# Kernel optimization log

Measured on AMD Instinct MI355X. Metric: run time of the kernel, lower is better.

## Reference

```python
import jax, jax.numpy as jnp
import numpy as np

B, N, H, M = 1, 1024, 64, 32


def _posenc(n, d):
    # sinusoidal positional encoding, matches torch PositionalEncoding (eval mode, no dropout)
    pos = jnp.arange(n, dtype=jnp.float32)[:, None]
    div = jnp.exp(jnp.arange(0, d, 2, dtype=jnp.float32) * (-np.log(10000.0) / d))
    ang = pos * div  # [n, d//2]
    pe = jnp.zeros((n, d), jnp.float32)
    pe = pe.at[:, 0::2].set(jnp.sin(ang))
    pe = pe.at[:, 1::2].set(jnp.cos(ang))
    return pe


def _egnn(x, h, m2f, w_msg, b_msg, w_pos, b_pos, w_feat, b_feat):
    # x: [B,N,3], h: [B,N,Hd], m2f: [B,N,N] float pair mask (diag zero)
    Bn, Nn, Hd = h.shape
    m2 = m2f[..., None]
    # r[b,i,j] = x[b,j] - x[b,i]  (torch: x.unsqueeze(-3) - x.unsqueeze(-2))
    r = (x[:, None, :, :] - x[:, :, None, :]) * m2  # [B,N,N,3]
    d2 = jnp.sum(r * r, axis=-1)  # [B,N,N]
    # message_mlp(cat(hi, hj, d2)): hi[b,i,j]=h[j], hj[b,i,j]=h[i]
    # split weight to avoid materializing the N x N x (2H+1) concat
    Wa, Wb, wd = w_msg[:, :Hd], w_msg[:, Hd:2 * Hd], w_msg[:, 2 * Hd]
    A = h @ Wa.T   # [B,N,M], contribution of h_j (hi slot)
    Bm = h @ Wb.T  # [B,N,M], contribution of h_i (hj slot)
    m = jax.nn.relu(A[:, None, :, :] + Bm[:, :, None, :] + d2[..., None] * wd + b_msg) * m2  # [B,N,N,M]
    mx = (m @ w_pos.T + b_pos) * r  # [B,N,N,3]
    x = x + jnp.sum(mx, axis=-2) / (Nn - 1)
    msum = jnp.sum(m, axis=-2)  # [B,N,M]
    h = jnp.concatenate([h, msum], axis=-1) @ w_feat.T + b_feat  # [B,N,Hd]
    return x, h


def setup_inputs() -> dict:
    key = jax.random.key(0)
    ks = jax.random.split(key, 16)
    def lin_w(k, o, i):
        return (jax.random.normal(k, (o, i), jnp.float32) / np.sqrt(i)).astype(jnp.float32)
    def lin_b(k, o):
        return (jax.random.normal(k, (o,), jnp.float32) * 0.02).astype(jnp.float32)
    return {
        'positions': jax.random.normal(ks[0], (B, N, 3), jnp.float32),
        'features': jax.random.normal(ks[1], (B, N, H), jnp.float32),
        'mask': jnp.ones((B, N), dtype=bool),
        'w_msg1': lin_w(ks[2], M, 2 * H + 1), 'b_msg1': lin_b(ks[3], M),
        'w_pos1': lin_w(ks[4], 3, M), 'b_pos1': lin_b(ks[5], 3),
        'w_feat1': lin_w(ks[6], H, M + H), 'b_feat1': lin_b(ks[7], H),
        'w_msg2': lin_w(ks[8], M, 2 * H + 1), 'b_msg2': lin_b(ks[9], M),
        'w_pos2': lin_w(ks[10], 3, M), 'b_pos2': lin_b(ks[11], 3),
        'w_feat2': lin_w(ks[12], H, M + H), 'b_feat2': lin_b(ks[13], H),
        't': 0,
    }


def reference(positions, features, mask,
              w_msg1, b_msg1, w_pos1, b_pos1, w_feat1, b_feat1,
              w_msg2, b_msg2, w_pos2, b_pos2, w_feat2, b_feat2, t):
    Bn, Nn, Hd = features.shape
    h = features + _posenc(Nn, Hd)[None]
    mask2 = mask[:, None, :] & mask[:, :, None]
    mask2 = mask2 & (~jnp.eye(Nn, dtype=bool))[None]  # zero self-pairs
    m2f = mask2.astype(positions.dtype)
    x = positions
    x, h = _egnn(x, h, m2f, w_msg1, b_msg1, w_pos1, b_pos1, w_feat1, b_feat1)
    h = jax.nn.relu(h)
    x, h = _egnn(x, h, m2f, w_msg2, b_msg2, w_pos2, b_pos2, w_feat2, b_feat2)
    return x
```

## Files before the change

### kernel.cpp

```cpp
#include <hip/hip_runtime.h>

#define N    1024
#define HD   64
#define MD   32
#define BLK  256
#define BLKP 512
#define WROW (2 * HD + 1)

typedef _Float16 h2 __attribute__((ext_vector_type(2)));

__device__ __forceinline__ float dot2(h2 a, h2 b, float c)
{
#if __has_builtin(__builtin_amdgcn_fdot2)
    return __builtin_amdgcn_fdot2(a, b, c, false);
#else
    return c + (float)a[0] * (float)b[0] + (float)a[1] * (float)b[1];
#endif
}
__device__ __forceinline__ h2 pack2(float x, float y)
{
    h2 r; r[0] = (_Float16)x; r[1] = (_Float16)y; return r;
}

__global__ __launch_bounds__(BLK) void k_p0(const float* __restrict__ feat,
                                            const float* __restrict__ wmsg,
                                            const float* __restrict__ bmsg,
                                            float* __restrict__ h0,
                                            float* __restrict__ A,
                                            float* __restrict__ Bb,
                                            _Float16* __restrict__ Ah)
{
    __shared__ float scr[4160 + 4 * HD];
    const int tid = threadIdx.x;
    const int n0  = blockIdx.x * 4;

    for (int u = tid; u < MD * WROW; u += BLK) scr[u] = wmsg[u];
    float* hrow = scr + 4160;
    {
        const int n = n0 + (tid >> 6), d = tid & 63;
        const float div = expf((float)(d & ~1) * (-9.210340371976184f / 64.0f));
        const float ang = (float)n * div;
        const float pe  = (d & 1) ? cosf(ang) : sinf(ang);
        const float hv  = feat[n * HD + d] + pe;
        h0[n * HD + d] = hv;
        hrow[tid] = hv;
    }
    __syncthreads();
    if (tid < 4 * MD) {
        const int nl = tid >> 5, m = tid & 31;
        const float* wa = scr + m * WROW;
        const float* hr = hrow + nl * HD;
        float sa = 0.f, sb = bmsg[m];
#pragma unroll
        for (int c = 0; c < HD; c++) {
            const float hv = hr[c];
            sa = fmaf(hv, wa[c], sa);
            sb = fmaf(hv, wa[HD + c], sb);
        }
        const int n = n0 + nl;
        A[n * MD + m]  = sa;
        Bb[n * MD + m] = sb;
        Ah[n * MD + m] = (_Float16)sa;
    }
}

template<int LAYER1>
__global__ __launch_bounds__(BLKP) void k_pair(
    const float* __restrict__ xsrc, const float* __restrict__ Aap,
    const _Float16* __restrict__ Ahp, const float* __restrict__ Bbp,
    const float* __restrict__ wmsg, const float* __restrict__ wpos,
    const float* __restrict__ bpos, float* __restrict__ xout,
    const float* __restrict__ h0, const float* __restrict__ wf,
    const float* __restrict__ bf, const float* __restrict__ wmsg2,
    const float* __restrict__ bmsg2, float* __restrict__ A2,
    float* __restrict__ B2, _Float16* __restrict__ A2h)
{
    const int tid   = threadIdx.x;
    const int wid   = tid >> 6;
    const int lane  = tid & 63;
    const int kq    = lane & 3;
    const int jslot = lane >> 2;

    __shared__ float  sbuf[6848];
    __shared__ float  wacc[8][8];
    __shared__ float  msAl[8][MD];
    __shared__ float  msBl[8][MD];
    __shared__ float  SxL[3];
    __shared__ float  msF[2][MD];
    __shared__ float  h0r[2][HD];
    __shared__ float  h1r[2][HD];
    float4* rd = (float4*)sbuf;

    const int iA = blockIdx.x, iB = blockIdx.x + N / 2;
    const float xiA0 = xsrc[iA * 3 + 0], xiA1 = xsrc[iA * 3 + 1], xiA2 = xsrc[iA * 3 + 2];
    const float xiB0 = xsrc[iB * 3 + 0], xiB1 = xsrc[iB * 3 + 1], xiB2 = xsrc[iB * 3 + 2];
    const float dx0 = xiA0 - xiB0, dx1 = xiA1 - xiB1, dx2 = xiA2 - xiB2;

    float sx0 = 0.f, sx1 = 0.f, sx2 = 0.f;
#pragma unroll
    for (int q = 0; q < N / BLKP; q++) {
        const int j = q * BLKP + tid;
        const float xj0 = xsrc[j * 3 + 0];
        const float xj1 = xsrc[j * 3 + 1];
        const float xj2 = xsrc[j * 3 + 2];
        sx0 += xj0; sx1 += xj1; sx2 += xj2;
        const float a0 = xj0 - xiA0, a1 = xj1 - xiA1, a2 = xj2 - xiA2;
        const float d2A = fmaf(a0, a0, fmaf(a1, a1, a2 * a2));
        const float b0 = xj0 - xiB0, b1 = xj1 - xiB1, b2 = xj2 - xiB2;
        const float d2B = fmaf(b0, b0, fmaf(b1, b1, b2 * b2));
        rd[j] = make_float4(a0, a1, a2, __builtin_bit_cast(float, pack2(d2A, d2B)));
    }
#pragma unroll
    for (int off = 32; off > 0; off >>= 1) {
        sx0 += __shfl_xor(sx0, off);
        sx1 += __shfl_xor(sx1, off);
        sx2 += __shfl_xor(sx2, off);
    }
    if (lane == 0) { wacc[wid][0] = sx0; wacc[wid][1] = sx1; wacc[wid][2] = sx2; }
    __syncthreads();
    if (tid == 0) {
        float s0 = 0.f, s1 = 0.f, s2 = 0.f;
#pragma unroll
        for (int w = 0; w < 8; w++) { s0 += wacc[w][0]; s1 += wacc[w][1]; s2 += wacc[w][2]; }
        SxL[0] = s0; SxL[1] = s1; SxL[2] = s2;
    }

    h2 biA[4], biB[4], wpx[4], wpy[4], wpz[4], wd[4];
    {
        const float4 bA0 = *(const float4*)(Bbp + iA * MD + kq * 8);
        const float4 bA1 = *(const float4*)(Bbp + iA * MD + kq * 8 + 4);
        const float4 bB0 = *(const float4*)(Bbp + iB * MD + kq * 8);
        const float4 bB1 = *(const float4*)(Bbp + iB * MD + kq * 8 + 4);
        biA[0] = pack2(bA0.x, bA0.y); biA[1] = pack2(bA0.z, bA0.w);
        biA[2] = pack2(bA1.x, bA1.y); biA[3] = pack2(bA1.z, bA1.w);
        biB[0] = pack2(bB0.x, bB0.y); biB[1] = pack2(bB0.z, bB0.w);
        biB[2] = pack2(bB1.x, bB1.y); biB[3] = pack2(bB1.z, bB1.w);
        const float4 px0 = *(const float4*)(wpos + kq * 8);
        const float4 px1 = *(const float4*)(wpos + kq * 8 + 4);
        const float4 py0 = *(const float4*)(wpos + MD + kq * 8);
        const float4 py1 = *(const float4*)(wpos + MD + kq * 8 + 4);
        const float4 pz0 = *(const float4*)(wpos + 2 * MD + kq * 8);
        const float4 pz1 = *(const float4*)(wpos + 2 * MD + kq * 8 + 4);
        wpx[0] = pack2(px0.x, px0.y); wpx[1] = pack2(px0.z, px0.w);
        wpx[2] = pack2(px1.x, px1.y); wpx[3] = pack2(px1.z, px1.w);
        wpy[0] = pack2(py0.x, py0.y); wpy[1] = pack2(py0.z, py0.w);
        wpy[2] = pack2(py1.x, py1.y); wpy[3] = pack2(py1.z, py1.w);
        wpz[0] = pack2(pz0.x, pz0.y); wpz[1] = pack2(pz0.z, pz0.w);
        wpz[2] = pack2(pz1.x, pz1.y); wpz[3] = pack2(pz1.z, pz1.w);
#pragma unroll
        for (int t = 0; t < 4; t++)
            wd[t] = pack2(wmsg[(kq * 8 + 2 * t) * WROW + 2 * HD],
                          wmsg[(kq * 8 + 2 * t + 1) * WROW + 2 * HD]);
    }
    const h2 hz = pack2(0.f, 0.f);

    float aA0 = 0.f, aA1 = 0.f, aA2 = 0.f, aB0 = 0.f, aB1 = 0.f, aB2 = 0.f;
    h2 msA[4] = {hz, hz, hz, hz}, msB[4] = {hz, hz, hz, hz};

    const int jb = wid * (N / 8);
#pragma unroll 8
    for (int it = 0; it < 8; it++) {
        const int j = jb + it * 16 + jslot;
        const uint4 au = *(const uint4*)(Ahp + j * MD + kq * 8);
        h2 a[4];
        a[0] = __builtin_bit_cast(h2, au.x); a[1] = __builtin_bit_cast(h2, au.y);
        a[2] = __builtin_bit_cast(h2, au.z); a[3] = __builtin_bit_cast(h2, au.w);
        const float4 f = rd[j];
        const h2 dd = __builtin_bit_cast(h2, f.w);
        const h2 dA = __builtin_shufflevector(dd, dd, 0, 0);
        const h2 dB = __builtin_shufflevector(dd, dd, 1, 1);
        const float rB0 = f.x + dx0, rB1 = f.y + dx1, rB2 = f.z + dx2;

        h2 mA[4], mB[4];
#pragma unroll
        for (int t = 0; t < 4; t++) {
            mA[t] = __builtin_elementwise_max(dA * wd[t] + (a[t] + biA[t]), hz);
            mB[t] = __builtin_elementwise_max(dB * wd[t] + (a[t] + biB[t]), hz);
            if (LAYER1) { msA[t] += mA[t]; msB[t] += mB[t]; }
        }
        const float sAx = dot2(mA[3], wpx[3], dot2(mA[2], wpx[2], dot2(mA[1], wpx[1], dot2(mA[0], wpx[0], 0.f))));
        const float sAy = dot2(mA[3], wpy[3], dot2(mA[2], wpy[2], dot2(mA[1], wpy[1], dot2(mA[0], wpy[0], 0.f))));
        const float sAz = dot2(mA[3], wpz[3], dot2(mA[2], wpz[2], dot2(mA[1], wpz[1], dot2(mA[0], wpz[0], 0.f))));
        const float sBx = dot2(mB[3], wpx[3], dot2(mB[2], wpx[2], dot2(mB[1], wpx[1], dot2(mB[0], wpx[0], 0.f))));
        const float sBy = dot2(mB[3], wpy[3], dot2(mB[2], wpy[2], dot2(mB[1], wpy[1], dot2(mB[0], wpy[0], 0.f))));
        const float sBz = dot2(mB[3], wpz[3], dot2(mB[2], wpz[2], dot2(mB[1], wpz[1], dot2(mB[0], wpz[0], 0.f))));
        aA0 = fmaf(sAx, f.x, aA0);
        aA1 = fmaf(sAy, f.y, aA1);
        aA2 = fmaf(sAz, f.z, aA2);
        aB0 = fmaf(sBx, rB0, aB0);
        aB1 = fmaf(sBy, rB1, aB1);
        aB2 = fmaf(sBz, rB2, aB2);
    }

#pragma unroll
    for (int off = 32; off > 0; off >>= 1) {
        aA0 += __shfl_xor(aA0, off); aA1 += __shfl_xor(aA1, off); aA2 += __shfl_xor(aA2, off);
        aB0 += __shfl_xor(aB0, off); aB1 += __shfl_xor(aB1, off); aB2 += __shfl_xor(aB2, off);
    }
    float msAf[8], msBf[8];
    if (LAYER1) {
#pragma unroll
        for (int t = 0; t < 4; t++) {
            msAf[2 * t] = (float)msA[t][0]; msAf[2 * t + 1] = (float)msA[t][1];
            msBf[2 * t] = (float)msB[t][0]; msBf[2 * t + 1] = (float)msB[t][1];
        }
#pragma unroll
        for (int off = 4; off <= 32; off <<= 1) {
#pragma unroll
            for (int t = 0; t < 8; t++) {
                msAf[t] += __shfl_xor(msAf[t], off);
                msBf[t] += __shfl_xor(msBf[t], off);
            }
        }
    }
    __syncthreads();
    if (lane == 0) {
        wacc[wid][0] = aA0; wacc[wid][1] = aA1; wacc[wid][2] = aA2;
        wacc[wid][3] = aB0; wacc[wid][4] = aB1; wacc[wid][5] = aB2;
    }
    if (LAYER1 && jslot == 0) {
#pragma unroll
        for (int t = 0; t < 8; t++) {
            msAl[wid][kq * 8 + t] = msAf[t];
            msBl[wid][kq * 8 + t] = msBf[t];
        }
    }
    __syncthreads();

    if (tid == 0) {
        const float bp0 = bpos[0], bp1 = bpos[1], bp2 = bpos[2];
        float vA0 = 0.f, vA1 = 0.f, vA2 = 0.f, vB0 = 0.f, vB1 = 0.f, vB2 = 0.f;
#pragma unroll
        for (int w = 0; w < 8; w++) {
            vA0 += wacc[w][0]; vA1 += wacc[w][1]; vA2 += wacc[w][2];
            vB0 += wacc[w][3]; vB1 += wacc[w][4]; vB2 += wacc[w][5];
        }
        const float inv = 1.0f / 1023.0f;
        xout[iA * 3 + 0] = xiA0 + (vA0 + bp0 * (SxL[0] - (float)N * xiA0)) * inv;
        xout[iA * 3 + 1] = xiA1 + (vA1 + bp1 * (SxL[1] - (float)N * xiA1)) * inv;
        xout[iA * 3 + 2] = xiA2 + (vA2 + bp2 * (SxL[2] - (float)N * xiA2)) * inv;
        xout[iB * 3 + 0] = xiB0 + (vB0 + bp0 * (SxL[0] - (float)N * xiB0)) * inv;
        xout[iB * 3 + 1] = xiB1 + (vB1 + bp1 * (SxL[1] - (float)N * xiB1)) * inv;
        xout[iB * 3 + 2] = xiB2 + (vB2 + bp2 * (SxL[2] - (float)N * xiB2)) * inv;
    }

    if (LAYER1) {
        float* scr = sbuf;
        if (tid < 2 * MD) {
            const int row = tid >> 5, k = tid & 31;
            const int i = row ? iB : iA;
            const float (*ml)[MD] = row ? msBl : msAl;
            float s = 0.f;
#pragma unroll
            for (int w = 0; w < 8; w++) s += ml[w][k];
            s -= fmaxf(Aap[i * MD + k] + Bbp[i * MD + k], 0.f);
            msF[row][k] = s;
        }
        for (int u = tid; u < HD * (HD + MD); u += BLKP) {
            const int o = u / (HD + MD), c = u - o * (HD + MD);
            scr[o * 97 + c] = wf[u];
        }
        if (tid < 2 * HD) {
            const int row = tid >> 6, d = tid & 63;
            h0r[row][d] = h0[(row ? iB : iA) * HD + d];
        }
        __syncthreads();
        if (tid < 2 * HD) {
            const int row = tid >> 6, o = tid & 63;
            const float* w = scr + o * 97;
            float s = bf[o];
#pragma unroll
            for (int c = 0; c < HD; c++) s = fmaf(h0r[row][c], w[c], s);
#pragma unroll
            for (int k = 0; k < MD; k++) s = fmaf(msF[row][k], w[HD + k], s);
            h1r[row][o] = fmaxf(s, 0.f);
        }
        __syncthreads();
        for (int u = tid; u < MD * WROW; u += BLKP) scr[u] = wmsg2[u];
        __syncthreads();
        if (tid < 2 * MD) {
            const int row = tid >> 5, m = tid & 31;
            const float* wa = scr + m * WROW;
            const float* hr = h1r[row];
            float sa = 0.f, sb = bmsg2[m];
#pragma unroll
            for (int c = 0; c < HD; c++) {
                const float hv = hr[c];
                sa = fmaf(hv, wa[c], sa);
                sb = fmaf(hv, wa[HD + c], sb);
            }
            const int i = row ? iB : iA;
            A2[i * MD + m]  = sa;
            B2[i * MD + m]  = sb;
            A2h[i * MD + m] = (_Float16)sa;
        }
    }
}

extern "C" void kernel_launch(void* const* d_in, const int* in_sizes, int n_in,
                              void* d_out, int out_size, void* d_ws, size_t ws_size,
                              hipStream_t stream)
{
    const float* pos     = (const float*)d_in[0];
    const float* feat    = (const float*)d_in[1];
    const float* w_msg1  = (const float*)d_in[3];
    const float* b_msg1  = (const float*)d_in[4];
    const float* w_pos1  = (const float*)d_in[5];
    const float* b_pos1  = (const float*)d_in[6];
    const float* w_feat1 = (const float*)d_in[7];
    const float* b_feat1 = (const float*)d_in[8];
    const float* w_msg2  = (const float*)d_in[9];
    const float* b_msg2  = (const float*)d_in[10];
    const float* w_pos2  = (const float*)d_in[11];
    const float* b_pos2  = (const float*)d_in[12];

    float* ws  = (float*)d_ws;
    float* h0  = ws;
    float* A1  = h0  + N * HD;
    float* B1  = A1  + N * MD;
    float* x1  = B1  + N * MD;
    float* A2  = x1  + N * 4;
    float* B2  = A2  + N * MD;
    _Float16* Ah1 = (_Float16*)(B2 + N * MD);
    _Float16* Ah2 = Ah1 + N * MD;

    k_p0<<<N / 4, BLK, 0, stream>>>(feat, w_msg1, b_msg1, h0, A1, B1, Ah1);
    k_pair<1><<<N / 2, BLKP, 0, stream>>>(pos, A1, Ah1, B1, w_msg1, w_pos1, b_pos1, x1,
                                          h0, w_feat1, b_feat1, w_msg2, b_msg2,
                                          A2, B2, Ah2);
    k_pair<0><<<N / 2, BLKP, 0, stream>>>(x1, A2, Ah2, B2, w_msg2, w_pos2, b_pos2,
                                          (float*)d_out,
                                          nullptr, nullptr, nullptr, nullptr,
                                          nullptr, nullptr, nullptr, nullptr);
}
```

Measured before the change: 33.68 us.

## Process four query rows per block in pair kernel with 1024-thread blocks

Each pair-kernel block now handles four i-rows instead of two and uses 1024 threads, halving the grid to 256 blocks. Each A_j load and each shared-memory rd read is reused across four rows, and the message sums are reduced in packed fp16 shuffles rather than fp32. This cuts global and LDS traffic per pair, but the larger blocks raise register pressure, and the grid now has only 256 blocks, which may leave CUs underused. The fp16 shuffle reductions also lower the precision of the message sums.

```diff
diff --git a/kernel.cpp b/kernel.cpp
--- a/kernel.cpp
+++ b/kernel.cpp
@@ -4,7 +4,7 @@
 #define HD   64
 #define MD   32
 #define BLK  256
-#define BLKP 512
+#define BLKP 1024
 #define WROW (2 * HD + 1)
 
 typedef _Float16 h2 __attribute__((ext_vector_type(2)));
@@ -82,59 +82,74 @@
     const int jslot = lane >> 2;
 
     __shared__ float  sbuf[6848];
-    __shared__ float  wacc[8][8];
-    __shared__ float  msAl[8][MD];
-    __shared__ float  msBl[8][MD];
+    __shared__ float  sxacc[16][3];
+    __shared__ float  vacc[16][4][3];
+    __shared__ float  msl[16][4][MD];
     __shared__ float  SxL[3];
-    __shared__ float  msF[2][MD];
-    __shared__ float  h0r[2][HD];
-    __shared__ float  h1r[2][HD];
-    float4* rd = (float4*)sbuf;
-
-    const int iA = blockIdx.x, iB = blockIdx.x + N / 2;
-    const float xiA0 = xsrc[iA * 3 + 0], xiA1 = xsrc[iA * 3 + 1], xiA2 = xsrc[iA * 3 + 2];
-    const float xiB0 = xsrc[iB * 3 + 0], xiB1 = xsrc[iB * 3 + 1], xiB2 = xsrc[iB * 3 + 2];
-    const float dx0 = xiA0 - xiB0, dx1 = xiA1 - xiB1, dx2 = xiA2 - xiB2;
-
-    float sx0 = 0.f, sx1 = 0.f, sx2 = 0.f;
-#pragma unroll
-    for (int q = 0; q < N / BLKP; q++) {
-        const int j = q * BLKP + tid;
+    __shared__ float  msF[4][MD];
+    __shared__ float  h0r[4][HD];
+    __shared__ float  h1r[4][HD];
+    float4*   rd  = (float4*)sbuf;
+    unsigned* ud2 = (unsigned*)(sbuf + 4096);
+
+    const int bb = blockIdx.x;
+    const int irow[4] = {bb, bb + 256, bb + 512, bb + 768};
+
+    float xi[4][3], dx[4][3];
+#pragma unroll
+    for (int r = 0; r < 4; r++)
+#pragma unroll
+        for (int c = 0; c < 3; c++) xi[r][c] = xsrc[irow[r] * 3 + c];
+#pragma unroll
+    for (int r = 0; r < 4; r++)
+#pragma unroll
+        for (int c = 0; c < 3; c++) dx[r][c] = xi[0][c] - xi[r][c];
+
+    {
+        const int j = tid;
         const float xj0 = xsrc[j * 3 + 0];
         const float xj1 = xsrc[j * 3 + 1];
         const float xj2 = xsrc[j * 3 + 2];
-        sx0 += xj0; sx1 += xj1; sx2 += xj2;
-        const float a0 = xj0 - xiA0, a1 = xj1 - xiA1, a2 = xj2 - xiA2;
-        const float d2A = fmaf(a0, a0, fmaf(a1, a1, a2 * a2));
-        const float b0 = xj0 - xiB0, b1 = xj1 - xiB1, b2 = xj2 - xiB2;
-        const float d2B = fmaf(b0, b0, fmaf(b1, b1, b2 * b2));
-        rd[j] = make_float4(a0, a1, a2, __builtin_bit_cast(float, pack2(d2A, d2B)));
-    }
-#pragma unroll
-    for (int off = 32; off > 0; off >>= 1) {
-        sx0 += __shfl_xor(sx0, off);
-        sx1 += __shfl_xor(sx1, off);
-        sx2 += __shfl_xor(sx2, off);
-    }
-    if (lane == 0) { wacc[wid][0] = sx0; wacc[wid][1] = sx1; wacc[wid][2] = sx2; }
+        float sx0 = xj0, sx1 = xj1, sx2 = xj2;
+        const float rA0 = xj0 - xi[0][0];
+        const float rA1 = xj1 - xi[0][1];
+        const float rA2 = xj2 - xi[0][2];
+        float d2v[4];
+#pragma unroll
+        for (int r = 0; r < 4; r++) {
+            const float r0 = rA0 + dx[r][0];
+            const float r1 = rA1 + dx[r][1];
+            const float r2 = rA2 + dx[r][2];
+            d2v[r] = fmaf(r0, r0, fmaf(r1, r1, r2 * r2));
+        }
+        rd[j]  = make_float4(rA0, rA1, rA2,
+                             __builtin_bit_cast(float, pack2(d2v[0], d2v[1])));
+        ud2[j] = __builtin_bit_cast(unsigned, pack2(d2v[2], d2v[3]));
+#pragma unroll
+        for (int off = 32; off > 0; off >>= 1) {
+            sx0 += __shfl_xor(sx0, off);
+            sx1 += __shfl_xor(sx1, off);
+            sx2 += __shfl_xor(sx2, off);
+        }
+        if (lane == 0) { sxacc[wid][0] = sx0; sxacc[wid][1] = sx1; sxacc[wid][2] = sx2; }
+    }
     __syncthreads();
     if (tid == 0) {
         float s0 = 0.f, s1 = 0.f, s2 = 0.f;
 #pragma unroll
-        for (int w = 0; w < 8; w++) { s0 += wacc[w][0]; s1 += wacc[w][1]; s2 += wacc[w][2]; }
+        for (int w = 0; w < 16; w++) { s0 += sxacc[w][0]; s1 += sxacc[w][1]; s2 += sxacc[w][2]; }
         SxL[0] = s0; SxL[1] = s1; SxL[2] = s2;
     }
 
-    h2 biA[4], biB[4], wpx[4], wpy[4], wpz[4], wd[4];
+    h2 bi[4][4], wpx[4], wpy[4], wpz[4], wd[4];
+#pragma unroll
+    for (int r = 0; r < 4; r++) {
+        const float4 b0 = *(const float4*)(Bbp + irow[r] * MD + kq * 8);
+        const float4 b1 = *(const float4*)(Bbp + irow[r] * MD + kq * 8 + 4);
+        bi[r][0] = pack2(b0.x, b0.y); bi[r][1] = pack2(b0.z, b0.w);
+        bi[r][2] = pack2(b1.x, b1.y); bi[r][3] = pack2(b1.z, b1.w);
+    }
     {
-        const float4 bA0 = *(const float4*)(Bbp + iA * MD + kq * 8);
-        const float4 bA1 = *(const float4*)(Bbp + iA * MD + kq * 8 + 4);
-        const float4 bB0 = *(const float4*)(Bbp + iB * MD + kq * 8);
-        const float4 bB1 = *(const float4*)(Bbp + iB * MD + kq * 8 + 4);
-        biA[0] = pack2(bA0.x, bA0.y); biA[1] = pack2(bA0.z, bA0.w);
-        biA[2] = pack2(bA1.x, bA1.y); biA[3] = pack2(bA1.z, bA1.w);
-        biB[0] = pack2(bB0.x, bB0.y); biB[1] = pack2(bB0.z, bB0.w);
-        biB[2] = pack2(bB1.x, bB1.y); biB[3] = pack2(bB1.z, bB1.w);
         const float4 px0 = *(const float4*)(wpos + kq * 8);
         const float4 px1 = *(const float4*)(wpos + kq * 8 + 4);
         const float4 py0 = *(const float4*)(wpos + MD + kq * 8);
@@ -154,105 +169,107 @@
     }
     const h2 hz = pack2(0.f, 0.f);
 
-    float aA0 = 0.f, aA1 = 0.f, aA2 = 0.f, aB0 = 0.f, aB1 = 0.f, aB2 = 0.f;
-    h2 msA[4] = {hz, hz, hz, hz}, msB[4] = {hz, hz, hz, hz};
-
-    const int jb = wid * (N / 8);
-#pragma unroll 8
-    for (int it = 0; it < 8; it++) {
+    float acc[4][3];
+    h2 ms[4][4];
+#pragma unroll
+    for (int r = 0; r < 4; r++) {
+        acc[r][0] = acc[r][1] = acc[r][2] = 0.f;
+        ms[r][0] = ms[r][1] = ms[r][2] = ms[r][3] = hz;
+    }
+
+    const int jb = wid * 64;
+#pragma unroll 4
+    for (int it = 0; it < 4; it++) {
         const int j = jb + it * 16 + jslot;
         const uint4 au = *(const uint4*)(Ahp + j * MD + kq * 8);
         h2 a[4];
         a[0] = __builtin_bit_cast(h2, au.x); a[1] = __builtin_bit_cast(h2, au.y);
         a[2] = __builtin_bit_cast(h2, au.z); a[3] = __builtin_bit_cast(h2, au.w);
         const float4 f = rd[j];
-        const h2 dd = __builtin_bit_cast(h2, f.w);
-        const h2 dA = __builtin_shufflevector(dd, dd, 0, 0);
-        const h2 dB = __builtin_shufflevector(dd, dd, 1, 1);
-        const float rB0 = f.x + dx0, rB1 = f.y + dx1, rB2 = f.z + dx2;
-
-        h2 mA[4], mB[4];
-#pragma unroll
-        for (int t = 0; t < 4; t++) {
-            mA[t] = __builtin_elementwise_max(dA * wd[t] + (a[t] + biA[t]), hz);
-            mB[t] = __builtin_elementwise_max(dB * wd[t] + (a[t] + biB[t]), hz);
-            if (LAYER1) { msA[t] += mA[t]; msB[t] += mB[t]; }
-        }
-        const float sAx = dot2(mA[3], wpx[3], dot2(mA[2], wpx[2], dot2(mA[1], wpx[1], dot2(mA[0], wpx[0], 0.f))));
-        const float sAy = dot2(mA[3], wpy[3], dot2(mA[2], wpy[2], dot2(mA[1], wpy[1], dot2(mA[0], wpy[0], 0.f))));
-        const float sAz = dot2(mA[3], wpz[3], dot2(mA[2], wpz[2], dot2(mA[1], wpz[1], dot2(mA[0], wpz[0], 0.f))));
-        const float sBx = dot2(mB[3], wpx[3], dot2(mB[2], wpx[2], dot2(mB[1], wpx[1], dot2(mB[0], wpx[0], 0.f))));
-        const float sBy = dot2(mB[3], wpy[3], dot2(mB[2], wpy[2], dot2(mB[1], wpy[1], dot2(mB[0], wpy[0], 0.f))));
-        const float sBz = dot2(mB[3], wpz[3], dot2(mB[2], wpz[2], dot2(mB[1], wpz[1], dot2(mB[0], wpz[0], 0.f))));
-        aA0 = fmaf(sAx, f.x, aA0);
-        aA1 = fmaf(sAy, f.y, aA1);
-        aA2 = fmaf(sAz, f.z, aA2);
-        aB0 = fmaf(sBx, rB0, aB0);
-        aB1 = fmaf(sBy, rB1, aB1);
-        aB2 = fmaf(sBz, rB2, aB2);
-    }
-
-#pragma unroll
-    for (int off = 32; off > 0; off >>= 1) {
-        aA0 += __shfl_xor(aA0, off); aA1 += __shfl_xor(aA1, off); aA2 += __shfl_xor(aA2, off);
-        aB0 += __shfl_xor(aB0, off); aB1 += __shfl_xor(aB1, off); aB2 += __shfl_xor(aB2, off);
-    }
-    float msAf[8], msBf[8];
+        const unsigned u23 = ud2[j];
+        const h2 dd01 = __builtin_bit_cast(h2, f.w);
+        const h2 dd23 = __builtin_bit_cast(h2, u23);
+        h2 d2s[4];
+        d2s[0] = __builtin_shufflevector(dd01, dd01, 0, 0);
+        d2s[1] = __builtin_shufflevector(dd01, dd01, 1, 1);
+        d2s[2] = __builtin_shufflevector(dd23, dd23, 0, 0);
+        d2s[3] = __builtin_shufflevector(dd23, dd23, 1, 1);
+
+#pragma unroll
+        for (int r = 0; r < 4; r++) {
+            const float r0 = (r == 0) ? f.x : f.x + dx[r][0];
+            const float r1 = (r == 0) ? f.y : f.y + dx[r][1];
+            const float r2 = (r == 0) ? f.z : f.z + dx[r][2];
+            h2 m[4];
+#pragma unroll
+            for (int t = 0; t < 4; t++) {
+                m[t] = __builtin_elementwise_max(d2s[r] * wd[t] + (a[t] + bi[r][t]), hz);
+                if (LAYER1) ms[r][t] += m[t];
+            }
+            const float sx = dot2(m[3], wpx[3], dot2(m[2], wpx[2], dot2(m[1], wpx[1], dot2(m[0], wpx[0], 0.f))));
+            const float sy = dot2(m[3], wpy[3], dot2(m[2], wpy[2], dot2(m[1], wpy[1], dot2(m[0], wpy[0], 0.f))));
+            const float sz = dot2(m[3], wpz[3], dot2(m[2], wpz[2], dot2(m[1], wpz[1], dot2(m[0], wpz[0], 0.f))));
+            acc[r][0] = fmaf(sx, r0, acc[r][0]);
+            acc[r][1] = fmaf(sy, r1, acc[r][1]);
+            acc[r][2] = fmaf(sz, r2, acc[r][2]);
+        }
+    }
+
+#pragma unroll
+    for (int off = 32; off > 0; off >>= 1)
+#pragma unroll
+        for (int r = 0; r < 4; r++) {
+            acc[r][0] += __shfl_xor(acc[r][0], off);
+            acc[r][1] += __shfl_xor(acc[r][1], off);
+            acc[r][2] += __shfl_xor(acc[r][2], off);
+        }
     if (LAYER1) {
 #pragma unroll
-        for (int t = 0; t < 4; t++) {
-            msAf[2 * t] = (float)msA[t][0]; msAf[2 * t + 1] = (float)msA[t][1];
-            msBf[2 * t] = (float)msB[t][0]; msBf[2 * t + 1] = (float)msB[t][1];
-        }
-#pragma unroll
-        for (int off = 4; off <= 32; off <<= 1) {
-#pragma unroll
-            for (int t = 0; t < 8; t++) {
-                msAf[t] += __shfl_xor(msAf[t], off);
-                msBf[t] += __shfl_xor(msBf[t], off);
+        for (int off = 4; off <= 32; off <<= 1)
+#pragma unroll
+            for (int r = 0; r < 4; r++)
+#pragma unroll
+                for (int t = 0; t < 4; t++) {
+                    const int v = __shfl_xor(__builtin_bit_cast(int, ms[r][t]), off);
+                    ms[r][t] += __builtin_bit_cast(h2, v);
+                }
+    }
+    if (lane == 0)
+#pragma unroll
+        for (int r = 0; r < 4; r++) {
+            vacc[wid][r][0] = acc[r][0];
+            vacc[wid][r][1] = acc[r][1];
+            vacc[wid][r][2] = acc[r][2];
+        }
+    if (LAYER1 && jslot == 0)
+#pragma unroll
+        for (int r = 0; r < 4; r++)
+#pragma unroll
+            for (int t = 0; t < 4; t++) {
+                msl[wid][r][kq * 8 + 2 * t]     = (float)ms[r][t][0];
+                msl[wid][r][kq * 8 + 2 * t + 1] = (float)ms[r][t][1];
             }
-        }
-    }
     __syncthreads();
-    if (lane == 0) {
-        wacc[wid][0] = aA0; wacc[wid][1] = aA1; wacc[wid][2] = aA2;
-        wacc[wid][3] = aB0; wacc[wid][4] = aB1; wacc[wid][5] = aB2;
-    }
-    if (LAYER1 && jslot == 0) {
-#pragma unroll
-        for (int t = 0; t < 8; t++) {
-            msAl[wid][kq * 8 + t] = msAf[t];
-            msBl[wid][kq * 8 + t] = msBf[t];
-        }
-    }
-    __syncthreads();
-
-    if (tid == 0) {
-        const float bp0 = bpos[0], bp1 = bpos[1], bp2 = bpos[2];
-        float vA0 = 0.f, vA1 = 0.f, vA2 = 0.f, vB0 = 0.f, vB1 = 0.f, vB2 = 0.f;
-#pragma unroll
-        for (int w = 0; w < 8; w++) {
-            vA0 += wacc[w][0]; vA1 += wacc[w][1]; vA2 += wacc[w][2];
-            vB0 += wacc[w][3]; vB1 += wacc[w][4]; vB2 += wacc[w][5];
-        }
-        const float inv = 1.0f / 1023.0f;
-        xout[iA * 3 + 0] = xiA0 + (vA0 + bp0 * (SxL[0] - (float)N * xiA0)) * inv;
-        xout[iA * 3 + 1] = xiA1 + (vA1 + bp1 * (SxL[1] - (float)N * xiA1)) * inv;
-        xout[iA * 3 + 2] = xiA2 + (vA2 + bp2 * (SxL[2] - (float)N * xiA2)) * inv;
-        xout[iB * 3 + 0] = xiB0 + (vB0 + bp0 * (SxL[0] - (float)N * xiB0)) * inv;
-        xout[iB * 3 + 1] = xiB1 + (vB1 + bp1 * (SxL[1] - (float)N * xiB1)) * inv;
-        xout[iB * 3 + 2] = xiB2 + (vB2 + bp2 * (SxL[2] - (float)N * xiB2)) * inv;
+
+    if (tid < 12) {
+        const int r = tid >> 2 == 0 ? tid / 3 : tid / 3;
+        const int rr = tid / 3, c = tid - rr * 3;
+        float a = 0.f;
+#pragma unroll
+        for (int w = 0; w < 16; w++) a += vacc[w][rr][c];
+        const int i = irow[rr];
+        const float x0 = xi[rr][c];
+        xout[i * 3 + c] = x0 + (a + bpos[c] * (SxL[c] - (float)N * x0)) * (1.0f / 1023.0f);
     }
 
     if (LAYER1) {
         float* scr = sbuf;
-        if (tid < 2 * MD) {
+        if (tid < 4 * MD) {
             const int row = tid >> 5, k = tid & 31;
-            const int i = row ? iB : iA;
-            const float (*ml)[MD] = row ? msBl : msAl;
+            const int i = irow[row];
             float s = 0.f;
 #pragma unroll
-            for (int w = 0; w < 8; w++) s += ml[w][k];
+            for (int w = 0; w < 16; w++) s += msl[w][row][k];
             s -= fmaxf(Aap[i * MD + k] + Bbp[i * MD + k], 0.f);
             msF[row][k] = s;
         }
@@ -260,12 +277,12 @@
             const int o = u / (HD + MD), c = u - o * (HD + MD);
             scr[o * 97 + c] = wf[u];
         }
-        if (tid < 2 * HD) {
+        if (tid < 4 * HD) {
             const int row = tid >> 6, d = tid & 63;
-            h0r[row][d] = h0[(row ? iB : iA) * HD + d];
+            h0r[row][d] = h0[irow[row] * HD + d];
         }
         __syncthreads();
-        if (tid < 2 * HD) {
+        if (tid < 4 * HD) {
             const int row = tid >> 6, o = tid & 63;
             const float* w = scr + o * 97;
             float s = bf[o];
@@ -278,7 +295,7 @@
         __syncthreads();
         for (int u = tid; u < MD * WROW; u += BLKP) scr[u] = wmsg2[u];
         __syncthreads();
-        if (tid < 2 * MD) {
+        if (tid < 4 * MD) {
             const int row = tid >> 5, m = tid & 31;
             const float* wa = scr + m * WROW;
             const float* hr = h1r[row];
@@ -289,7 +306,7 @@
                 sa = fmaf(hv, wa[c], sa);
                 sb = fmaf(hv, wa[HD + c], sb);
             }
-            const int i = row ? iB : iA;
+            const int i = irow[row];
             A2[i * MD + m]  = sa;
             B2[i * MD + m]  = sb;
             A2h[i * MD + m] = (_Float16)sa;
@@ -325,10 +342,10 @@
     _Float16* Ah2 = Ah1 + N * MD;
 
     k_p0<<<N / 4, BLK, 0, stream>>>(feat, w_msg1, b_msg1, h0, A1, B1, Ah1);
-    k_pair<1><<<N / 2, BLKP, 0, stream>>>(pos, A1, Ah1, B1, w_msg1, w_pos1, b_pos1, x1,
+    k_pair<1><<<N / 4, BLKP, 0, stream>>>(pos, A1, Ah1, B1, w_msg1, w_pos1, b_pos1, x1,
                                           h0, w_feat1, b_feat1, w_msg2, b_msg2,
                                           A2, B2, Ah2);
-    k_pair<0><<<N / 2, BLKP, 0, stream>>>(x1, A2, Ah2, B2, w_msg2, w_pos2, b_pos2,
+    k_pair<0><<<N / 4, BLKP, 0, stream>>>(x1, A2, Ah2, B2, w_msg2, w_pos2, b_pos2,
                                           (float*)d_out,
                                           nullptr, nullptr, nullptr, nullptr,
                                           nullptr, nullptr, nullptr, nullptr);
```

After: 67.50 us. 100% more time.
